# Optimization experiments

Measured on AMD Instinct MI355X. Metric: run time of the kernel, lower is better.

## Reference

```python
import jax, jax.numpy as jnp
from jax import lax
import numpy as np

B, T, CENC, EMB, H, HH, NL, P, NTAG = 16, 512, 128, 512, 512, 256, 2, 8, 12


def _cell(x, h, c, Wih, Whh, bih, bhh):
    # torch LSTM gate order: i, f, g, o
    g = x @ Wih.T + h @ Whh.T + bih + bhh
    i, f, gg, o = jnp.split(g, 4, axis=-1)
    c = jax.nn.sigmoid(f) * c + jax.nn.sigmoid(i) * jnp.tanh(gg)
    h = jax.nn.sigmoid(o) * jnp.tanh(c)
    return h, c


def _masked_scan(xs, mask, h0, c0, p):
    # xs [T,B,D], mask [T,B,1]; packed-sequence semantics: state frozen and
    # output zeroed at padded steps (matches pack/pad_packed with sorted lens).
    def step(carry, inp):
        h, c = carry
        x, m = inp
        h2, c2 = _cell(x, h, c, *p)
        h = jnp.where(m > 0, h2, h)
        c = jnp.where(m > 0, c2, c)
        return (h, c), h * m
    _, out = lax.scan(step, (h0, c0), (xs, mask))
    return out  # [T,B,HH]


def _rev_within(x, lens):
    # reverse each sequence within its own length (positions >= len get junk,
    # which callers re-mask to zero)
    t = jnp.arange(x.shape[0])[:, None]
    idx = jnp.clip(lens[None, :] - 1 - t, 0)
    return jnp.take_along_axis(x, jnp.broadcast_to(idx[:, :, None], x.shape), axis=0)


def _seg_scan(u, p, forward):
    # u [B,T,H]. Fused batched segment scan over all (batch, position) streams.
    # forward:  step k feeds token s+k to stream s  -> out[k][b,s] = LSTM(u[s..s+k])
    # backward: step k feeds token t-k to stream t  -> out[k][b,t] = LSTM(u[t],u[t-1],..,u[t-k])
    pad = ((0, 0), (0, P), (0, 0)) if forward else ((0, 0), (P, 0), (0, 0))
    upad = jnp.pad(u, pad)
    h0 = jnp.zeros((u.shape[0], u.shape[1], HH), u.dtype)
    def step(carry, k):
        h, c = carry
        start = k if forward else P - k
        x = lax.dynamic_slice_in_dim(upad, start, u.shape[1], axis=1)
        h, c = _cell(x, h, c, *p)
        return (h, c), h
    _, out = lax.scan(step, (h0, h0), jnp.arange(P))
    return out  # [P,B,T,HH]


def _forward(lens, x, h0, c0, W_emb, b_emb, Wih, Whh, bih, bhh,
             Wih_sf, Whh_sf, bih_sf, bhh_sf, Wih_sr, Whh_sr, bih_sr, bhh_sr,
             Wfc, bfc):
    mask = (jnp.arange(T)[:, None] < lens[None, :]).astype(x.dtype)[:, :, None]  # [T,B,1]
    inp = x @ W_emb.T + b_emb  # char_embed (dropout is identity in eval / p=0)
    for l in range(NL):  # 2-layer bidirectional encoder LSTM
        pf = (Wih[2 * l], Whh[2 * l], bih[2 * l], bhh[2 * l])
        pr = (Wih[2 * l + 1], Whh[2 * l + 1], bih[2 * l + 1], bhh[2 * l + 1])
        of = _masked_scan(inp, mask, h0[2 * l], c0[2 * l], pf)
        orv = _masked_scan(_rev_within(inp, lens), mask, h0[2 * l + 1], c0[2 * l + 1], pr)
        orv = _rev_within(orv, lens) * mask
        inp = jnp.concatenate([of, orv], axis=-1)
    u = inp.transpose(1, 0, 2)  # [B,T,H] (== `unpacked` transposed)
    out_f = _seg_scan(u, (Wih_sf, Whh_sf, bih_sf, bhh_sf), True)
    out_r = _seg_scan(u, (Wih_sr, Whh_sr, bih_sr, bhh_sr), False)
    t = jnp.arange(T)[:, None]
    i = jnp.arange(P)[None, :]
    s = jnp.clip(t - i, 0)  # segment start = t - i
    ib = jnp.broadcast_to(i, (T, P))
    # segment_feat_fwd[b,t,i] = fwd LSTM over tokens t-i..t  (= out_f[i, b, t-i])
    seg_f = out_f[ib, :, s].transpose(2, 0, 1, 3)  # [B,T,P,HH]
    # segment_feat_rev[b,t,i] = rev LSTM over tokens t..t-i  (= out_r[i, b, t])
    seg_r = out_r.transpose(1, 2, 0, 3)  # [B,T,P,HH]
    valid = (t >= i)[None, :, :, None] & (jnp.arange(T)[None, :, None, None] < lens[:, None, None, None])
    seg = jnp.concatenate([seg_f, seg_r], axis=-1) * valid.astype(x.dtype)
    return seg @ Wfc.T + bfc  # [B,T,P,NTAG]; fc(0)=bias at unwritten slots, as in torch


def setup_inputs():
    key = jax.random.key(0)
    ks = jax.random.split(key, 12)
    def uni(k, shape):
        r = float(np.sqrt(6.0 / sum(shape)))
        return jax.random.uniform(k, shape, jnp.float32, -r, r)
    x = jax.random.normal(ks[0], (T, B, CENC), jnp.float32)
    lens = jnp.sort(jax.random.randint(ks[1], (B,), T // 2, T + 1))[::-1]
    lens = lens.at[0].set(T)  # descending, max == T (pack_padded requirement)
    z = jnp.zeros
    return {
        "x": x,
        "h0": z((2 * NL, B, HH), jnp.float32),
        "c0": z((2 * NL, B, HH), jnp.float32),
        "W_emb": uni(ks[2], (EMB, CENC)), "b_emb": z((EMB,), jnp.float32),
        "Wih": uni(ks[3], (2 * NL, 4 * HH, H)), "Whh": uni(ks[4], (2 * NL, 4 * HH, HH)),
        "bih": z((2 * NL, 4 * HH), jnp.float32), "bhh": z((2 * NL, 4 * HH), jnp.float32),
        "Wih_sf": uni(ks[5], (4 * HH, H)), "Whh_sf": uni(ks[6], (4 * HH, HH)),
        "bih_sf": z((4 * HH,), jnp.float32), "bhh_sf": z((4 * HH,), jnp.float32),
        "Wih_sr": uni(ks[7], (4 * HH, H)), "Whh_sr": uni(ks[8], (4 * HH, HH)),
        "bih_sr": z((4 * HH,), jnp.float32), "bhh_sr": z((4 * HH,), jnp.float32),
        "Wfc": uni(ks[9], (NTAG, H)), "bfc": z((NTAG,), jnp.float32),
        "lens": lens,
    }


def reference(x, h0, c0, W_emb, b_emb, Wih, Whh, bih, bhh, Wih_sf, Whh_sf,
              bih_sf, bhh_sf, Wih_sr, Whh_sr, bih_sr, bhh_sr, Wfc, bfc, lens):
    return _forward(lens, x, h0, c0, W_emb, b_emb, Wih, Whh, bih, bhh,
                    Wih_sf, Whh_sf, bih_sf, bhh_sf, Wih_sr, Whh_sr, bih_sr, bhh_sr,
                    Wfc, bfc)
```

## Files before the change

kernel.cpp:

```cpp
#include <hip/hip_runtime.h>
#include <math.h>

#define Bn    16
#define Tn    512
#define CENCn 128
#define EMBn  512
#define Hn    512
#define HHn   256
#define Pn    8
#define NTAGn 12
#define G4n   1024

__device__ __forceinline__ float sigm(float x) { return 1.f / (1.f + expf(-x)); }

__global__ __launch_bounds__(256) void gemm_tn(
    const float* __restrict__ A, const float* __restrict__ Bm,
    float* __restrict__ C, const float* __restrict__ b1,
    const float* __restrict__ b2, int M, int N, int K)
{
    __shared__ float As[16][132];
    __shared__ float Bs[16][132];
    const int tid = threadIdx.x;
    const int tx = tid & 15, ty = tid >> 4;
    const int m0 = blockIdx.y * 128, n0 = blockIdx.x * 128;

    float acc[8][8];
#pragma unroll
    for (int i = 0; i < 8; i++)
#pragma unroll
        for (int j = 0; j < 8; j++) acc[i][j] = 0.f;

    const int r  = tid >> 2;
    const int cc = (tid & 3) * 4;

    for (int k0 = 0; k0 < K; k0 += 16) {
#pragma unroll
        for (int hh = 0; hh < 2; hh++) {
            const int row = r + hh * 64;
            const float4 va = *(const float4*)(A + (size_t)(m0 + row) * K + k0 + cc);
            As[cc + 0][row] = va.x; As[cc + 1][row] = va.y;
            As[cc + 2][row] = va.z; As[cc + 3][row] = va.w;
            const float4 vb = *(const float4*)(Bm + (size_t)(n0 + row) * K + k0 + cc);
            Bs[cc + 0][row] = vb.x; Bs[cc + 1][row] = vb.y;
            Bs[cc + 2][row] = vb.z; Bs[cc + 3][row] = vb.w;
        }
        __syncthreads();
#pragma unroll
        for (int kk = 0; kk < 16; kk++) {
            const float4 a0 = *(const float4*)&As[kk][ty * 4];
            const float4 a1 = *(const float4*)&As[kk][64 + ty * 4];
            const float4 b0 = *(const float4*)&Bs[kk][tx * 4];
            const float4 b1v = *(const float4*)&Bs[kk][64 + tx * 4];
            const float av[8] = {a0.x, a0.y, a0.z, a0.w, a1.x, a1.y, a1.z, a1.w};
            const float bv[8] = {b0.x, b0.y, b0.z, b0.w, b1v.x, b1v.y, b1v.z, b1v.w};
#pragma unroll
            for (int ii = 0; ii < 8; ii++)
#pragma unroll
                for (int jj = 0; jj < 8; jj++) acc[ii][jj] += av[ii] * bv[jj];
        }
        __syncthreads();
    }

    float bb[8];
#pragma unroll
    for (int jj = 0; jj < 8; jj++) {
        const int col = n0 + ((jj < 4) ? (tx * 4 + jj) : (64 + tx * 4 + jj - 4));
        bb[jj] = (b1 ? b1[col] : 0.f) + (b2 ? b2[col] : 0.f);
    }
#pragma unroll
    for (int ii = 0; ii < 8; ii++) {
        const int row = m0 + ((ii < 4) ? (ty * 4 + ii) : (64 + ty * 4 + ii - 4));
        float4 v0, v1;
        v0.x = acc[ii][0] + bb[0]; v0.y = acc[ii][1] + bb[1];
        v0.z = acc[ii][2] + bb[2]; v0.w = acc[ii][3] + bb[3];
        v1.x = acc[ii][4] + bb[4]; v1.y = acc[ii][5] + bb[5];
        v1.z = acc[ii][6] + bb[6]; v1.w = acc[ii][7] + bb[7];
        *(float4*)(C + (size_t)row * N + n0 + tx * 4) = v0;
        *(float4*)(C + (size_t)row * N + n0 + 64 + tx * 4) = v1;
    }
}

__global__ __launch_bounds__(256) void enc_step(
    const float* __restrict__ Gf, const float* __restrict__ Gr,
    const float* __restrict__ WhhF, const float* __restrict__ WhhR,
    float* __restrict__ h_ws, float* __restrict__ c_ws,
    float* __restrict__ outbuf, const int* __restrict__ lens, int t)
{
    __shared__ float wsh[32][257];
    __shared__ float hsh[16][256];
    __shared__ float gsh[512];
    const int tid = threadIdx.x;
    const int dir = blockIdx.x >> 5;
    const int g   = blockIdx.x & 31;
    const float* Whh = dir ? WhhR : WhhF;
    const float* Gx  = dir ? Gr : Gf;

#pragma unroll
    for (int i = 0; i < 8; i++) {
        const int f4 = i * 256 + tid;
        const int r32 = f4 >> 6;
        const int kc = (f4 & 63) * 4;
        const int q = r32 >> 3, hdl = r32 & 7;
        const float4 v = *(const float4*)(Whh + (size_t)(g * 8 + hdl + (q << 8)) * HHn + kc);
        wsh[r32][kc + 0] = v.x; wsh[r32][kc + 1] = v.y;
        wsh[r32][kc + 2] = v.z; wsh[r32][kc + 3] = v.w;
    }
#pragma unroll
    for (int i = 0; i < 4; i++) {
        const int f4 = i * 256 + tid;
        const int b = f4 >> 6;
        const int kc = (f4 & 63) * 4;
        *(float4*)&hsh[b][kc] = *(const float4*)(h_ws + ((dir * 16 + b) << 8) + kc);
    }
    __syncthreads();

    const int b0 = tid >> 5, r0 = tid & 31;
    float acc0 = 0.f, acc1 = 0.f;
#pragma unroll 8
    for (int k = 0; k < 256; k++) {
        const float wv = wsh[r0][k];
        acc0 += hsh[b0][k] * wv;
        acc1 += hsh[b0 + 8][k] * wv;
    }
    {
        const int q = r0 >> 3, hdl = r0 & 7;
        const int j = g * 8 + hdl + (q << 8);
        const int lb0 = lens[b0], lb1 = lens[b0 + 8];
        const int idx0 = dir ? max(lb0 - 1 - t, 0) : t;
        const int idx1 = dir ? max(lb1 - 1 - t, 0) : t;
        gsh[(b0 << 5) + r0]       = acc0 + Gx[(size_t)(idx0 * Bn + b0) * G4n + j];
        gsh[((b0 + 8) << 5) + r0] = acc1 + Gx[(size_t)(idx1 * Bn + b0 + 8) * G4n + j];
    }
    __syncthreads();

    if (tid < 128) {
        const int b = tid >> 3, hdl = tid & 7;
        const int lb = lens[b];
        if (t < lb) {
            const int hd = g * 8 + hdl;
            const float gi = gsh[(b << 5) + hdl];
            const float gf = gsh[(b << 5) + 8 + hdl];
            const float gg = gsh[(b << 5) + 16 + hdl];
            const float go = gsh[(b << 5) + 24 + hdl];
            const int sidx = ((dir * 16 + b) << 8) + hd;
            const float c_new = sigm(gf) * c_ws[sidx] + sigm(gi) * tanhf(gg);
            const float h_new = sigm(go) * tanhf(c_new);
            h_ws[sidx] = h_new;
            c_ws[sidx] = c_new;
            const int trow = dir ? (lb - 1 - t) : t;
            outbuf[(size_t)(trow * Bn + b) * Hn + dir * HHn + hd] = h_new;
        }
    }
}

__global__ __launch_bounds__(256) void seg_cell(
    const float* __restrict__ GT, const float* __restrict__ Gx,
    float* __restrict__ Hs, float* __restrict__ Cs,
    const float* __restrict__ Wfc, float* __restrict__ outp,
    const int* __restrict__ lens, int k, int dir)
{
    __shared__ float hshs[256];
    const int s = blockIdx.x;
    const int b = s >> 9, t0 = s & 511;
    const int tid = threadIdx.x;
    const int tau = dir ? (t0 - k) : (t0 + k);
    const int tauc = min(max(tau, 0), Tn - 1);
    const size_t grow = ((size_t)(b << 9) + tauc) * G4n;
    const size_t srow = (size_t)s * G4n;

    const float gi = GT[srow + tid]       + Gx[grow + tid];
    const float gf = GT[srow + 256 + tid] + Gx[grow + 256 + tid];
    const float gg = GT[srow + 512 + tid] + Gx[grow + 512 + tid];
    const float go = GT[srow + 768 + tid] + Gx[grow + 768 + tid];
    const size_t hidx = (size_t)s * 256 + tid;
    const float c_new = sigm(gf) * Cs[hidx] + sigm(gi) * tanhf(gg);
    const float h_new = sigm(go) * tanhf(c_new);
    Cs[hidx] = c_new;
    Hs[hidx] = h_new;
    hshs[tid] = h_new;
    __syncthreads();

    const int t_out = dir ? t0 : (t0 + k);
    const bool valid = dir ? (t0 >= k && t0 < lens[b])
                           : (t_out < Tn && t_out < lens[b]);
    if (valid && tid < 192) {
        const int n = tid >> 4, l = tid & 15;
        const int off = dir ? 256 : 0;
        float a = 0.f;
#pragma unroll
        for (int e = 0; e < 16; e++)
            a += hshs[l + (e << 4)] * Wfc[n * Hn + off + l + (e << 4)];
        a += __shfl_down(a, 8, 16);
        a += __shfl_down(a, 4, 16);
        a += __shfl_down(a, 2, 16);
        a += __shfl_down(a, 1, 16);
        if (l == 0) {
            const size_t oidx = (((size_t)(b << 9) + t_out) * Pn + k) * NTAGn + n;
            outp[oidx] += a;
        }
    }
}

__global__ __launch_bounds__(256) void transpose_tb(
    const float* __restrict__ in, float* __restrict__ outp)
{
    const int s = blockIdx.x;
    const int b = s >> 9, t = s & 511;
    const int tid = threadIdx.x;
    const float* src = in + (size_t)(t * Bn + b) * Hn;
    float* dst = outp + (size_t)s * Hn;
    dst[tid] = src[tid];
    dst[tid + 256] = src[tid + 256];
}

__global__ __launch_bounds__(256) void init_out(
    float* __restrict__ outp, const float* __restrict__ bfc, int n)
{
    const int i = blockIdx.x * 256 + threadIdx.x;
    if (i < n) outp[i] = bfc[i % NTAGn];
}

extern "C" void kernel_launch(void* const* d_in, const int* in_sizes, int n_in,
                              void* d_out, int out_size, void* d_ws, size_t ws_size,
                              hipStream_t stream)
{
    (void)in_sizes; (void)n_in; (void)out_size; (void)ws_size;
    const float* x      = (const float*)d_in[0];
    const float* h0     = (const float*)d_in[1];
    const float* c0     = (const float*)d_in[2];
    const float* W_emb  = (const float*)d_in[3];
    const float* b_emb  = (const float*)d_in[4];
    const float* Wih    = (const float*)d_in[5];
    const float* Whh    = (const float*)d_in[6];
    const float* bih    = (const float*)d_in[7];
    const float* bhh    = (const float*)d_in[8];
    const float* Wih_sf = (const float*)d_in[9];
    const float* Whh_sf = (const float*)d_in[10];
    const float* bih_sf = (const float*)d_in[11];
    const float* bhh_sf = (const float*)d_in[12];
    const float* Wih_sr = (const float*)d_in[13];
    const float* Whh_sr = (const float*)d_in[14];
    const float* bih_sr = (const float*)d_in[15];
    const float* bhh_sr = (const float*)d_in[16];
    const float* Wfc    = (const float*)d_in[17];
    const float* bfc    = (const float*)d_in[18];
    const int*   lens   = (const int*)d_in[19];
    float* out = (float*)d_out;
    float* w   = (float*)d_ws;

    float* bufA = w;
    float* bufB = w + 4194304;
    float* G0   = w + 8388608;
    float* G1   = w + 16777216;
    float* U    = w + 25165824;
    float* Hs   = w + 29360128;
    float* Cs   = w + 31457280;
    float* h_ws = w + 33554432;
    float* c_ws = w + 33562624;
    float* GT   = w;

    const dim3 blk(256);

    gemm_tn<<<dim3(EMBn / 128, (Tn * Bn) / 128), blk, 0, stream>>>(
        x, W_emb, bufA, b_emb, nullptr, Tn * Bn, EMBn, CENCn);

    for (int l = 0; l < 2; l++) {
        const float* Xin = l ? bufB : bufA;
        float* O = l ? bufA : bufB;
        const float* WihF = Wih + (size_t)(2 * l) * G4n * Hn;
        const float* WihR = Wih + (size_t)(2 * l + 1) * G4n * Hn;
        const float* WhhF = Whh + (size_t)(2 * l) * G4n * HHn;
        const float* WhhR = Whh + (size_t)(2 * l + 1) * G4n * HHn;
        gemm_tn<<<dim3(G4n / 128, 64), blk, 0, stream>>>(
            Xin, WihF, G0, bih + (size_t)(2 * l) * G4n, bhh + (size_t)(2 * l) * G4n,
            Tn * Bn, G4n, Hn);
        gemm_tn<<<dim3(G4n / 128, 64), blk, 0, stream>>>(
            Xin, WihR, G1, bih + (size_t)(2 * l + 1) * G4n, bhh + (size_t)(2 * l + 1) * G4n,
            Tn * Bn, G4n, Hn);
        hipMemsetAsync(O, 0, (size_t)4194304 * 4, stream);
        hipMemcpyAsync(h_ws, h0 + (size_t)(2 * l) * Bn * HHn, (size_t)2 * Bn * HHn * 4,
                       hipMemcpyDeviceToDevice, stream);
        hipMemcpyAsync(c_ws, c0 + (size_t)(2 * l) * Bn * HHn, (size_t)2 * Bn * HHn * 4,
                       hipMemcpyDeviceToDevice, stream);
        for (int t = 0; t < Tn; t++)
            enc_step<<<64, blk, 0, stream>>>(G0, G1, WhhF, WhhR, h_ws, c_ws, O, lens, t);
    }

    transpose_tb<<<Bn * Tn, blk, 0, stream>>>(bufA, U);

    gemm_tn<<<dim3(G4n / 128, 64), blk, 0, stream>>>(
        U, Wih_sf, G0, bih_sf, bhh_sf, Bn * Tn, G4n, Hn);
    gemm_tn<<<dim3(G4n / 128, 64), blk, 0, stream>>>(
        U, Wih_sr, G1, bih_sr, bhh_sr, Bn * Tn, G4n, Hn);

    init_out<<<(Bn * Tn * Pn * NTAGn + 255) / 256, blk, 0, stream>>>(
        out, bfc, Bn * Tn * Pn * NTAGn);

    for (int dir = 0; dir < 2; dir++) {
        const float* Whh_s = dir ? Whh_sr : Whh_sf;
        const float* Gx = dir ? G1 : G0;
        hipMemsetAsync(Hs, 0, (size_t)2097152 * 4, stream);
        hipMemsetAsync(Cs, 0, (size_t)2097152 * 4, stream);
        for (int k = 0; k < Pn; k++) {
            if (k == 0)
                hipMemsetAsync(GT, 0, (size_t)8388608 * 4, stream);
            else
                gemm_tn<<<dim3(G4n / 128, 64), blk, 0, stream>>>(
                    Hs, Whh_s, GT, nullptr, nullptr, Bn * Tn, G4n, HHn);
            seg_cell<<<Bn * Tn, blk, 0, stream>>>(GT, Gx, Hs, Cs, Wfc, out, lens, k, dir);
        }
    }
}
```

Measured before the change: 9.167 ms.

## Replace per-timestep encoder launches with persistent scan kernel using grid barrier

The 512 per-timestep enc_step launches per layer become one persistent kernel of 64 blocks. Each block keeps its slice of the recurrent weights in registers, exchanges h through a double-buffered global array, and synchronises with a software atomic barrier. The forward and reverse input projections are merged into one GEMM with N=2048. The segment-scan memsets are dropped by special-casing k==0, and sigmoid/tanh use fast __expf. The risks are spin-barrier latency, the requirement that all 64 blocks be co-resident, and reduced accuracy from the fast exp approximations.

```diff
diff --git a/kernel.cpp b/kernel.cpp
--- a/kernel.cpp
+++ b/kernel.cpp
@@ -11,7 +11,8 @@
 #define NTAGn 12
 #define G4n   1024
 
-__device__ __forceinline__ float sigm(float x) { return 1.f / (1.f + expf(-x)); }
+__device__ __forceinline__ float sigm(float x) { return 1.f / (1.f + __expf(-x)); }
+__device__ __forceinline__ float tanh_(float x) { return 2.f / (1.f + __expf(-2.f * x)) - 1.f; }
 
 __global__ __launch_bounds__(256) void gemm_tn(
     const float* __restrict__ A, const float* __restrict__ Bm,
@@ -80,76 +81,143 @@
     }
 }
 
-__global__ __launch_bounds__(256) void enc_step(
-    const float* __restrict__ Gf, const float* __restrict__ Gr,
-    const float* __restrict__ WhhF, const float* __restrict__ WhhR,
-    float* __restrict__ h_ws, float* __restrict__ c_ws,
-    float* __restrict__ outbuf, const int* __restrict__ lens, int t)
-{
-    __shared__ float wsh[32][257];
-    __shared__ float hsh[16][256];
-    __shared__ float gsh[512];
+__device__ __forceinline__ void bar_sync(unsigned* cnt, unsigned* gen, unsigned nblk)
+{
+    __syncthreads();
+    if (threadIdx.x == 0) {
+        unsigned g0 = __hip_atomic_load(gen, __ATOMIC_RELAXED, __HIP_MEMORY_SCOPE_AGENT);
+        unsigned a  = __hip_atomic_fetch_add(cnt, 1u, __ATOMIC_ACQ_REL, __HIP_MEMORY_SCOPE_AGENT);
+        if (a + 1u == nblk) {
+            __hip_atomic_store(cnt, 0u, __ATOMIC_RELAXED, __HIP_MEMORY_SCOPE_AGENT);
+            __hip_atomic_fetch_add(gen, 1u, __ATOMIC_RELEASE, __HIP_MEMORY_SCOPE_AGENT);
+        } else {
+            unsigned gg;
+            do {
+                __builtin_amdgcn_s_sleep(2);
+                gg = __hip_atomic_load(gen, __ATOMIC_ACQUIRE, __HIP_MEMORY_SCOPE_AGENT);
+            } while (gg == g0);
+        }
+    }
+    __syncthreads();
+}
+
+__global__ __launch_bounds__(256, 1) void enc_scan(
+    const float* __restrict__ Gx, const float* __restrict__ WhhF,
+    const float* __restrict__ WhhR, const float* __restrict__ h0_l,
+    const float* __restrict__ c0_l, float* __restrict__ outbuf,
+    const int* __restrict__ lens, float* __restrict__ hx,
+    unsigned* __restrict__ bar)
+{
+    __shared__ float hsh[16 * 288];
+    __shared__ float psh[32 * 129];
     const int tid = threadIdx.x;
     const int dir = blockIdx.x >> 5;
     const int g   = blockIdx.x & 31;
     const float* Whh = dir ? WhhR : WhhF;
-    const float* Gx  = dir ? Gr : Gf;
-
-#pragma unroll
-    for (int i = 0; i < 8; i++) {
-        const int f4 = i * 256 + tid;
-        const int r32 = f4 >> 6;
-        const int kc = (f4 & 63) * 4;
-        const int q = r32 >> 3, hdl = r32 & 7;
-        const float4 v = *(const float4*)(Whh + (size_t)(g * 8 + hdl + (q << 8)) * HHn + kc);
-        wsh[r32][kc + 0] = v.x; wsh[r32][kc + 1] = v.y;
-        wsh[r32][kc + 2] = v.z; wsh[r32][kc + 3] = v.w;
-    }
-#pragma unroll
-    for (int i = 0; i < 4; i++) {
-        const int f4 = i * 256 + tid;
-        const int b = f4 >> 6;
-        const int kc = (f4 & 63) * 4;
-        *(float4*)&hsh[b][kc] = *(const float4*)(h_ws + ((dir * 16 + b) << 8) + kc);
-    }
-    __syncthreads();
-
-    const int b0 = tid >> 5, r0 = tid & 31;
-    float acc0 = 0.f, acc1 = 0.f;
-#pragma unroll 8
-    for (int k = 0; k < 256; k++) {
-        const float wv = wsh[r0][k];
-        acc0 += hsh[b0][k] * wv;
-        acc1 += hsh[b0 + 8][k] * wv;
-    }
-    {
-        const int q = r0 >> 3, hdl = r0 & 7;
-        const int j = g * 8 + hdl + (q << 8);
-        const int lb0 = lens[b0], lb1 = lens[b0 + 8];
-        const int idx0 = dir ? max(lb0 - 1 - t, 0) : t;
-        const int idx1 = dir ? max(lb1 - 1 - t, 0) : t;
-        gsh[(b0 << 5) + r0]       = acc0 + Gx[(size_t)(idx0 * Bn + b0) * G4n + j];
-        gsh[((b0 + 8) << 5) + r0] = acc1 + Gx[(size_t)(idx1 * Bn + b0 + 8) * G4n + j];
-    }
-    __syncthreads();
-
+    unsigned* cnt = bar + dir * 32;
+    unsigned* gen = bar + dir * 32 + 16;
+
+    const int kc = tid & 7;
+    const int rw = (tid >> 3) & 7;
+    const int bs = tid >> 6;
+
+    float4 w4[32];
+#pragma unroll
+    for (int ri = 0; ri < 4; ri++) {
+        const int lr = rw * 4 + ri;
+        const int grow = ((lr >> 3) << 8) + g * 8 + (lr & 7);
+#pragma unroll
+        for (int j4 = 0; j4 < 8; j4++)
+            w4[ri * 8 + j4] = *(const float4*)(Whh + (size_t)grow * HHn + kc * 32 + j4 * 4);
+    }
+
+    const int cb = tid >> 3, cj = tid & 7;
+    const int hd = g * 8 + cj;
+    float h_reg = 0.f, c_reg = 0.f;
+    int lb = 0;
     if (tid < 128) {
-        const int b = tid >> 3, hdl = tid & 7;
-        const int lb = lens[b];
-        if (t < lb) {
-            const int hd = g * 8 + hdl;
-            const float gi = gsh[(b << 5) + hdl];
-            const float gf = gsh[(b << 5) + 8 + hdl];
-            const float gg = gsh[(b << 5) + 16 + hdl];
-            const float go = gsh[(b << 5) + 24 + hdl];
-            const int sidx = ((dir * 16 + b) << 8) + hd;
-            const float c_new = sigm(gf) * c_ws[sidx] + sigm(gi) * tanhf(gg);
-            const float h_new = sigm(go) * tanhf(c_new);
-            h_ws[sidx] = h_new;
-            c_ws[sidx] = c_new;
+        lb = lens[cb];
+        h_reg = h0_l[dir * 4096 + cb * 256 + hd];
+        c_reg = c0_l[dir * 4096 + cb * 256 + hd];
+    }
+
+    const int hpos_k = (tid >> 5) * 36 + (tid & 31);
+
+    for (int t = 0; t < Tn; t++) {
+        float gx0 = 0.f, gx1 = 0.f, gx2 = 0.f, gx3 = 0.f;
+        const bool act = (tid < 128) && (t < lb);
+        if (act) {
+            const int tr_in = dir ? (lb - 1 - t) : t;
+            const size_t gbase = ((size_t)tr_in * Bn + cb) * 2048 + dir * 1024 + g * 8 + cj;
+            gx0 = Gx[gbase];
+            gx1 = Gx[gbase + 256];
+            gx2 = Gx[gbase + 512];
+            gx3 = Gx[gbase + 768];
+        }
+
+        if (t == 0) {
+#pragma unroll
+            for (int i = 0; i < 16; i++)
+                hsh[i * 288 + hpos_k] = h0_l[dir * 4096 + i * 256 + tid];
+        } else {
+            const float* src = hx + (((t - 1) & 1) * 8192) + dir * 4096;
+#pragma unroll
+            for (int i = 0; i < 16; i++)
+                hsh[i * 288 + hpos_k] =
+                    __hip_atomic_load(src + i * 256 + tid, __ATOMIC_RELAXED,
+                                      __HIP_MEMORY_SCOPE_AGENT);
+        }
+        __syncthreads();
+
+        float acc[4][4];
+#pragma unroll
+        for (int bl = 0; bl < 4; bl++) {
+            const int b = bs * 4 + bl;
+            const float4* hrow = (const float4*)(hsh + b * 288 + kc * 36);
+            float4 hv[8];
+#pragma unroll
+            for (int j4 = 0; j4 < 8; j4++) hv[j4] = hrow[j4];
+#pragma unroll
+            for (int ri = 0; ri < 4; ri++) {
+                float s = 0.f;
+#pragma unroll
+                for (int j4 = 0; j4 < 8; j4++) {
+                    const float4 wv = w4[ri * 8 + j4];
+                    s += wv.x * hv[j4].x + wv.y * hv[j4].y
+                       + wv.z * hv[j4].z + wv.w * hv[j4].w;
+                }
+                acc[ri][bl] = s;
+            }
+        }
+#pragma unroll
+        for (int ri = 0; ri < 4; ri++)
+#pragma unroll
+            for (int bl = 0; bl < 4; bl++)
+                psh[(rw * 4 + ri) * 129 + (bs * 4 + bl) * 8 + kc] = acc[ri][bl];
+        __syncthreads();
+
+        if (act) {
+            float s0 = gx0, s1 = gx1, s2 = gx2, s3 = gx3;
+            const int pb = cb * 8;
+#pragma unroll
+            for (int kcc = 0; kcc < 8; kcc++) {
+                s0 += psh[(0 * 8 + cj) * 129 + pb + kcc];
+                s1 += psh[(1 * 8 + cj) * 129 + pb + kcc];
+                s2 += psh[(2 * 8 + cj) * 129 + pb + kcc];
+                s3 += psh[(3 * 8 + cj) * 129 + pb + kcc];
+            }
+            const float c_new = sigm(s1) * c_reg + sigm(s0) * tanh_(s2);
+            const float h_new = sigm(s3) * tanh_(c_new);
+            c_reg = c_new;
+            h_reg = h_new;
             const int trow = dir ? (lb - 1 - t) : t;
-            outbuf[(size_t)(trow * Bn + b) * Hn + dir * HHn + hd] = h_new;
-        }
+            outbuf[((size_t)trow * Bn + cb) * Hn + dir * HHn + hd] = h_new;
+        }
+        if (tid < 128)
+            __hip_atomic_store(hx + ((t & 1) * 8192) + dir * 4096 + cb * 256 + hd,
+                               h_reg, __ATOMIC_RELAXED, __HIP_MEMORY_SCOPE_AGENT);
+
+        if (t != Tn - 1) bar_sync(cnt, gen, 32u);
     }
 }
 
@@ -167,14 +235,22 @@
     const int tauc = min(max(tau, 0), Tn - 1);
     const size_t grow = ((size_t)(b << 9) + tauc) * G4n;
     const size_t srow = (size_t)s * G4n;
-
-    const float gi = GT[srow + tid]       + Gx[grow + tid];
-    const float gf = GT[srow + 256 + tid] + Gx[grow + 256 + tid];
-    const float gg = GT[srow + 512 + tid] + Gx[grow + 512 + tid];
-    const float go = GT[srow + 768 + tid] + Gx[grow + 768 + tid];
     const size_t hidx = (size_t)s * 256 + tid;
-    const float c_new = sigm(gf) * Cs[hidx] + sigm(gi) * tanhf(gg);
-    const float h_new = sigm(go) * tanhf(c_new);
+
+    float gi = Gx[grow + tid];
+    float gf = Gx[grow + 256 + tid];
+    float gg = Gx[grow + 512 + tid];
+    float go = Gx[grow + 768 + tid];
+    float cprev = 0.f;
+    if (k > 0) {
+        gi += GT[srow + tid];
+        gf += GT[srow + 256 + tid];
+        gg += GT[srow + 512 + tid];
+        go += GT[srow + 768 + tid];
+        cprev = Cs[hidx];
+    }
+    const float c_new = sigm(gf) * cprev + sigm(gi) * tanh_(gg);
+    const float h_new = sigm(go) * tanh_(c_new);
     Cs[hidx] = c_new;
     Hs[hidx] = h_new;
     hshs[tid] = h_new;
@@ -255,8 +331,9 @@
     float* U    = w + 25165824;
     float* Hs   = w + 29360128;
     float* Cs   = w + 31457280;
-    float* h_ws = w + 33554432;
-    float* c_ws = w + 33562624;
+    float* hx   = w + 33554432;
+    unsigned* bar = (unsigned*)(w + 33570816);
+    float* Gbig = G0;
     float* GT   = w;
 
     const dim3 blk(256);
@@ -267,23 +344,17 @@
     for (int l = 0; l < 2; l++) {
         const float* Xin = l ? bufB : bufA;
         float* O = l ? bufA : bufB;
-        const float* WihF = Wih + (size_t)(2 * l) * G4n * Hn;
-        const float* WihR = Wih + (size_t)(2 * l + 1) * G4n * Hn;
-        const float* WhhF = Whh + (size_t)(2 * l) * G4n * HHn;
-        const float* WhhR = Whh + (size_t)(2 * l + 1) * G4n * HHn;
-        gemm_tn<<<dim3(G4n / 128, 64), blk, 0, stream>>>(
-            Xin, WihF, G0, bih + (size_t)(2 * l) * G4n, bhh + (size_t)(2 * l) * G4n,
-            Tn * Bn, G4n, Hn);
-        gemm_tn<<<dim3(G4n / 128, 64), blk, 0, stream>>>(
-            Xin, WihR, G1, bih + (size_t)(2 * l + 1) * G4n, bhh + (size_t)(2 * l + 1) * G4n,
-            Tn * Bn, G4n, Hn);
+        gemm_tn<<<dim3(2048 / 128, 64), blk, 0, stream>>>(
+            Xin, Wih + (size_t)(2 * l) * G4n * Hn, Gbig,
+            bih + (size_t)(2 * l) * G4n, bhh + (size_t)(2 * l) * G4n,
+            Tn * Bn, 2048, Hn);
         hipMemsetAsync(O, 0, (size_t)4194304 * 4, stream);
-        hipMemcpyAsync(h_ws, h0 + (size_t)(2 * l) * Bn * HHn, (size_t)2 * Bn * HHn * 4,
-                       hipMemcpyDeviceToDevice, stream);
-        hipMemcpyAsync(c_ws, c0 + (size_t)(2 * l) * Bn * HHn, (size_t)2 * Bn * HHn * 4,
-                       hipMemcpyDeviceToDevice, stream);
-        for (int t = 0; t < Tn; t++)
-            enc_step<<<64, blk, 0, stream>>>(G0, G1, WhhF, WhhR, h_ws, c_ws, O, lens, t);
+        hipMemsetAsync(bar, 0, 64 * sizeof(unsigned), stream);
+        enc_scan<<<64, blk, 0, stream>>>(
+            Gbig,
+            Whh + (size_t)(2 * l) * G4n * HHn, Whh + (size_t)(2 * l + 1) * G4n * HHn,
+            h0 + (size_t)l * 8192, c0 + (size_t)l * 8192,
+            O, lens, hx, bar);
     }
 
     transpose_tb<<<Bn * Tn, blk, 0, stream>>>(bufA, U);
@@ -299,12 +370,8 @@
     for (int dir = 0; dir < 2; dir++) {
         const float* Whh_s = dir ? Whh_sr : Whh_sf;
         const float* Gx = dir ? G1 : G0;
-        hipMemsetAsync(Hs, 0, (size_t)2097152 * 4, stream);
-        hipMemsetAsync(Cs, 0, (size_t)2097152 * 4, stream);
         for (int k = 0; k < Pn; k++) {
-            if (k == 0)
-                hipMemsetAsync(GT, 0, (size_t)8388608 * 4, stream);
-            else
+            if (k > 0)
                 gemm_tn<<<dim3(G4n / 128, 64), blk, 0, stream>>>(
                     Hs, Whh_s, GT, nullptr, nullptr, Bn * Tn, G4n, HHn);
             seg_cell<<<Bn * Tn, blk, 0, stream>>>(GT, Gx, Hs, Cs, Wfc, out, lens, k, dir);
```

Result: slower. 11.96 ms (+30.5%).
